# Kernel optimization log

Hardware: AMD Instinct MI355X
Metric: run time of the kernel (lower is better)

The kernel has to match this reference:

```python
import jax, jax.numpy as jnp
import numpy as np
from jax import lax

B, T = 8192, 128
HID = 64


def setup_inputs() -> dict:
    key = jax.random.key(0)
    ks = jax.random.split(key, 16)
    actor_ids = jax.random.randint(ks[0], (B, T), 0, 7, dtype=jnp.int32)
    action_ids = jax.random.randint(ks[1], (B, T), 0, 4, dtype=jnp.int32)
    street_ids = jax.random.randint(ks[2], (B, T), 0, 5, dtype=jnp.int32)
    bet_fraction = jax.random.uniform(ks[3], (B, T, 1), dtype=jnp.float32)
    # prefix-valid mask from random lengths (some zero-length rows)
    lengths = jax.random.randint(ks[4], (B,), 0, T + 1)
    valid_mask = jnp.arange(T)[None, :] < lengths[:, None]  # [B,T] bool
    s = 0.1
    params = {
        "E_actor": jax.random.normal(ks[5], (7, 8), jnp.float32) * s,
        "E_action": jax.random.normal(ks[6], (4, 8), jnp.float32) * s,
        "E_street": jax.random.normal(ks[7], (5, 4), jnp.float32) * s,
        "W_proj": jax.random.normal(ks[8], (32, 21), jnp.float32) * s,
        "b_proj": jax.random.normal(ks[9], (32,), jnp.float32) * s,
        "W_ih": jax.random.normal(ks[10], (3 * HID, 32), jnp.float32) * s,
        "W_hh": jax.random.normal(ks[11], (3 * HID, HID), jnp.float32) * s,
        "b_ih": jax.random.normal(ks[12], (3 * HID,), jnp.float32) * s,
        "b_hh": jax.random.normal(ks[13], (3 * HID,), jnp.float32) * s,
    }
    return dict(actor_ids=actor_ids, action_ids=action_ids, street_ids=street_ids,
                bet_fraction=bet_fraction, valid_mask=valid_mask, **params)


def reference(actor_ids, action_ids, street_ids, bet_fraction, valid_mask,
              E_actor, E_action, E_street, W_proj, b_proj,
              W_ih, W_hh, b_ih, b_hh):
    # embed + concat -> [B,T,21]
    feats = jnp.concatenate([E_actor[actor_ids], E_action[action_ids],
                             E_street[street_ids], bet_fraction], axis=-1)
    x = feats @ W_proj.T + b_proj                      # [B,T,32]
    # precompute input-side GRU gates for all timesteps: [B,T,3H]
    xg = x @ W_ih.T + b_ih
    xg_t = jnp.swapaxes(xg, 0, 1)                      # [T,B,3H]
    m_t = jnp.swapaxes(valid_mask, 0, 1)               # [T,B]

    def step(h, inp):
        xg_i, m = inp
        hg = h @ W_hh.T + b_hh                         # [B,3H]
        xr, xz, xn = jnp.split(xg_i, 3, axis=-1)
        hr, hz, hn = jnp.split(hg, 3, axis=-1)
        r = jax.nn.sigmoid(xr + hr)
        z = jax.nn.sigmoid(xz + hz)
        n = jnp.tanh(xn + r * hn)
        h_new = (1.0 - z) * n + z * h
        # only advance hidden state while t < length (prefix-valid mask);
        # final carry equals the GRU hidden at the last valid step, and rows
        # with length 0 stay at the zero init (matches torch masking).
        h = jnp.where(m[:, None], h_new, h)
        return h, None

    h0 = jnp.zeros((x.shape[0], HID), dtype=x.dtype)
    h_final, _ = lax.scan(step, h0, (xg_t, m_t))
    return h_final
```

## Files before the change

### kernel.cpp

```cpp
#include <hip/hip_runtime.h>

#define HID 64
#define TT  128
#define NROWS 8192
#define NGRP (NROWS / 16)
#define LOG2E 1.44269504088896f

typedef _Float16 half8 __attribute__((ext_vector_type(8)));
typedef float    f32x4 __attribute__((ext_vector_type(4)));

#define WS_WF    0
#define WS_WHH   12288
#define WS_BA    36864
#define WS_BX    37376
#define WS_BH    37632
#define WS_EMB   37888
#define WS_LROW  38176
#define WS_ORDER 70944

__global__ __launch_bounds__(256) void prep(
    const float* __restrict__ E_actor, const float* __restrict__ E_action,
    const float* __restrict__ E_street, const float* __restrict__ W_proj,
    const float* __restrict__ b_proj, const float* __restrict__ W_ih,
    const float* __restrict__ b_ih, const float* __restrict__ W_hh,
    const float* __restrict__ b_hh, const int* __restrict__ mask,
    char* __restrict__ ws)
{
    const int j = threadIdx.x;
    if (blockIdx.x != 64) {
        int* Lrow = (int*)(ws + WS_LROW);
        const int wv = j >> 6, ln = j & 63;
        const int r0 = blockIdx.x * 128;
        for (int i = 0; i < 32; i++) {
            const int row = r0 + i * 4 + wv, base = row * TT;
            const int m0 = mask[base + ln], m1 = mask[base + 64 + ln];
            const int L = __popcll(__ballot(m0 != 0)) + __popcll(__ballot(m1 != 0));
            if (ln == 0) Lrow[row] = L;
        }
        return;
    }

    _Float16* WF  = (_Float16*)(ws + WS_WF);
    _Float16* WHH = (_Float16*)(ws + WS_WHH);
    float*    BA  = (float*)(ws + WS_BA);
    float*    BX  = (float*)(ws + WS_BX);
    float*    BH  = (float*)(ws + WS_BH);
    _Float16* EMB = (_Float16*)(ws + WS_EMB);

    __shared__ float wfs[192][32];
    if (j < 192) {
        float wf[21];
        #pragma unroll
        for (int m = 0; m < 21; m++) wf[m] = 0.f;
        float bf = b_ih[j];
        for (int k = 0; k < 32; k++) {
            float w = W_ih[j * 32 + k];
            bf += w * b_proj[k];
            #pragma unroll
            for (int m = 0; m < 21; m++) wf[m] += w * W_proj[k * 21 + m];
        }
        const float s = (j < 128) ? LOG2E : 2.f * LOG2E;
        #pragma unroll
        for (int m = 0; m < 21; m++) wfs[j][m] = wf[m] * s;
        #pragma unroll
        for (int m = 21; m < 32; m++) wfs[j][m] = 0.f;
        if (j < 128) BA[j] = (bf + b_hh[j]) * LOG2E;
        else { BX[j - 128] = bf * 2.f * LOG2E; BH[j - 128] = b_hh[j] * 2.f * LOG2E; }
    }
    if (j < 17 * 8) {
        int r = j >> 3, m = j & 7;
        float v = 0.f;
        if (r < 7)       v = E_actor[r * 8 + m];
        else if (r < 11) v = E_action[(r - 7) * 8 + m];
        else if (r < 16) v = (m < 4) ? E_street[(r - 11) * 4 + m] : 0.f;
        EMB[j] = (_Float16)v;
    }
    __syncthreads();

    for (int idx = j; idx < 12 * 64; idx += 256) {
        const int T = idx >> 6, lane = idx & 63;
        const int g3 = T >> 2, w = T & 3, m16 = lane & 15, kq = lane >> 4;
        const int jr = g3 * 64 + w * 16 + m16;
        _Float16 v[8];
        #pragma unroll
        for (int m = 0; m < 8; m++) v[m] = (_Float16)wfs[jr][kq * 8 + m];
        *(uint4*)&WF[idx * 8] = *(uint4*)v;
    }
    for (int idx = j; idx < 12 * 2 * 64; idx += 256) {
        const int T = idx >> 7, rem = idx & 127, kt = rem >> 6, lane = rem & 63;
        const int g3 = T >> 2, w = T & 3, m16 = lane & 15, kq = lane >> 4;
        const int jr = g3 * 64 + w * 16 + m16;
        const int kbase = kt * 32 + kq * 8;
        const float s = (jr < 128) ? LOG2E : 2.f * LOG2E;
        _Float16 v[8];
        #pragma unroll
        for (int m = 0; m < 8; m++) v[m] = (_Float16)(W_hh[jr * HID + kbase + m] * s);
        *(uint4*)&WHH[((T * 2 + kt) * 64 + lane) * 8] = *(uint4*)v;
    }
}

__global__ __launch_bounds__(256) void sort_rows(
    const int* __restrict__ Lrow, int* __restrict__ order)
{
    __shared__ int hist[TT + 1];
    __shared__ int pref[TT + 1];
    const int tid = threadIdx.x;
    if (tid <= TT) hist[tid] = 0;
    __syncthreads();
    int rnk[NROWS / 256], Ls[NROWS / 256];
    #pragma unroll 4
    for (int i = 0; i < NROWS / 256; i++) {
        const int r = i * 256 + tid;
        const int L = Lrow[r];
        Ls[i] = L;
        rnk[i] = atomicAdd(&hist[L], 1);
    }
    __syncthreads();
    if (tid == 0) {
        int run = 0;
        for (int i = 0; i <= TT; i++) { pref[i] = run; run += hist[i]; }
    }
    __syncthreads();
    #pragma unroll 4
    for (int i = 0; i < NROWS / 256; i++) {
        const int r = i * 256 + tid;
        order[pref[Ls[i]] + rnk[i]] = r;
    }
}

__global__ __launch_bounds__(256, 2) void gru_mfma(
    const int* __restrict__ actor_ids, const int* __restrict__ action_ids,
    const int* __restrict__ street_ids, const float* __restrict__ bet,
    const char* __restrict__ ws, const int* __restrict__ order,
    const int* __restrict__ Lrow, float* __restrict__ out)
{
    const _Float16* WF  = (const _Float16*)(ws + WS_WF);
    const _Float16* WHH = (const _Float16*)(ws + WS_WHH);
    const float*    BA  = (const float*)(ws + WS_BA);
    const float*    BX  = (const float*)(ws + WS_BX);
    const float*    BH  = (const float*)(ws + WS_BH);
    const _Float16* EMB = (const _Float16*)(ws + WS_EMB);

    __shared__ int pb[TT][17];
    __shared__ __align__(16) _Float16 hb[2][16][72];
    __shared__ __align__(16) _Float16 embl[144];

    const int tid = threadIdx.x;
    const int wv  = tid >> 6;
    const int l   = tid & 63;
    const int q   = l >> 4;
    const int n   = l & 15;

    const int b = blockIdx.x;
    const int g = (b & 1) ? (NGRP - 1 - (b >> 1)) : (b >> 1);

    for (int i = tid; i < 136; i += 256) embl[i] = EMB[i];
    for (int i = tid; i < 2 * 16 * 72 / 2; i += 256) ((int*)hb)[i] = 0;
    {
        const int r = tid >> 4, tl = tid & 15;
        const int rowr = order[g * 16 + r];
        const int base = rowr * TT;
        #pragma unroll
        for (int i = 0; i < 8; i++) {
            const int t = tl + 16 * i;
            const int a = actor_ids[base + t], c = action_ids[base + t];
            const int s = street_ids[base + t];
            const _Float16 f16 = (_Float16)bet[base + t];
            const unsigned fb = (unsigned)*(const unsigned short*)&f16;
            pb[t][r] = (int)(a | (c << 3) | (s << 5) | (fb << 16));
        }
    }

    half8 Af[3], Ah[3][2];
    #pragma unroll
    for (int g3 = 0; g3 < 3; g3++) {
        const int T = g3 * 4 + wv;
        Af[g3]    = *(const half8*)&WF[(T * 64 + l) * 8];
        Ah[g3][0] = *(const half8*)&WHH[((T * 2 + 0) * 64 + l) * 8];
        Ah[g3][1] = *(const half8*)&WHH[((T * 2 + 1) * 64 + l) * 8];
    }
    f32x4 biasR, biasZ, biasX, biasH;
    #pragma unroll
    for (int e = 0; e < 4; e++) {
        const int idx = 16 * wv + 4 * q + e;
        biasR[e] = BA[idx];
        biasZ[e] = BA[64 + idx];
        biasX[e] = BX[idx];
        biasH[e] = BH[idx];
    }

    const int myrow = order[g * 16 + n];
    const int Ln    = Lrow[myrow];
    const int Lmax  = __shfl(Ln, 15);
    const bool isq2 = (q == 2);
    const int sh = (q == 1) ? 3 : (q == 2) ? 5 : 0;
    const int mk = (q == 1) ? 3 : (q == 3) ? 0 : 7;
    const int of = (q == 1) ? 7 : (q == 2) ? 11 : (q == 3) ? 16 : 0;

    float h[4] = {0.f, 0.f, 0.f, 0.f};

    __syncthreads();

    f32x4 xR, xZ, xX;
    {
        const int p = pb[0][n];
        const int eidx = ((p >> sh) & mk) + of;
        half8 Bf = *(const half8*)&embl[eidx * 8];
        uint4* bu = (uint4*)&Bf;
        bu->z = isq2 ? ((unsigned)p >> 16) : bu->z;
        xR = __builtin_amdgcn_mfma_f32_16x16x32_f16(Af[0], Bf, biasR, 0, 0, 0);
        xZ = __builtin_amdgcn_mfma_f32_16x16x32_f16(Af[1], Bf, biasZ, 0, 0, 0);
        xX = __builtin_amdgcn_mfma_f32_16x16x32_f16(Af[2], Bf, biasX, 0, 0, 0);
    }

    for (int t = 0; t < Lmax; t++) {
        const int buf = t & 1;
        const half8 Bh0 = *(const half8*)&hb[buf][n][q * 8];
        const half8 Bh1 = *(const half8*)&hb[buf][n][32 + q * 8];
        f32x4 aR = __builtin_amdgcn_mfma_f32_16x16x32_f16(Ah[0][0], Bh0, xR, 0, 0, 0);
        aR = __builtin_amdgcn_mfma_f32_16x16x32_f16(Ah[0][1], Bh1, aR, 0, 0, 0);
        f32x4 aZ = __builtin_amdgcn_mfma_f32_16x16x32_f16(Ah[1][0], Bh0, xZ, 0, 0, 0);
        aZ = __builtin_amdgcn_mfma_f32_16x16x32_f16(Ah[1][1], Bh1, aZ, 0, 0, 0);
        f32x4 aH = __builtin_amdgcn_mfma_f32_16x16x32_f16(Ah[2][0], Bh0, biasH, 0, 0, 0);
        aH = __builtin_amdgcn_mfma_f32_16x16x32_f16(Ah[2][1], Bh1, aH, 0, 0, 0);
        const f32x4 aXc = xX;

        {
            const int tn = (t + 1 < TT) ? t + 1 : TT - 1;
            const int p = pb[tn][n];
            const int eidx = ((p >> sh) & mk) + of;
            half8 Bf = *(const half8*)&embl[eidx * 8];
            uint4* bu = (uint4*)&Bf;
            bu->z = isq2 ? ((unsigned)p >> 16) : bu->z;
            xR = __builtin_amdgcn_mfma_f32_16x16x32_f16(Af[0], Bf, biasR, 0, 0, 0);
            xZ = __builtin_amdgcn_mfma_f32_16x16x32_f16(Af[1], Bf, biasZ, 0, 0, 0);
            xX = __builtin_amdgcn_mfma_f32_16x16x32_f16(Af[2], Bf, biasX, 0, 0, 0);
        }

        const bool live = (t < Ln);
        _Float16 hp[4];
        #pragma unroll
        for (int e = 0; e < 4; e++) {
            const float r = __builtin_amdgcn_rcpf(1.f + __builtin_amdgcn_exp2f(-aR[e]));
            const float z = __builtin_amdgcn_rcpf(1.f + __builtin_amdgcn_exp2f(-aZ[e]));
            const float y2 = aXc[e] + r * aH[e];
            const float nn = 1.f - 2.f * __builtin_amdgcn_rcpf(1.f + __builtin_amdgcn_exp2f(y2));
            const float hv = nn + z * (h[e] - nn);
            h[e] = live ? hv : h[e];
            hp[e] = (_Float16)h[e];
        }
        *(uint2*)&hb[buf ^ 1][n][16 * wv + 4 * q] = *(uint2*)hp;
        __syncthreads();
    }

    float4 o = make_float4(h[0], h[1], h[2], h[3]);
    *(float4*)&out[myrow * HID + 16 * wv + 4 * q] = o;
}

extern "C" void kernel_launch(void* const* d_in, const int* in_sizes, int n_in,
                              void* d_out, int out_size, void* d_ws, size_t ws_size,
                              hipStream_t stream) {
    const int*   actor_ids  = (const int*)d_in[0];
    const int*   action_ids = (const int*)d_in[1];
    const int*   street_ids = (const int*)d_in[2];
    const float* bet        = (const float*)d_in[3];
    const int*   vmask      = (const int*)d_in[4];
    const float* E_actor    = (const float*)d_in[5];
    const float* E_action   = (const float*)d_in[6];
    const float* E_street   = (const float*)d_in[7];
    const float* W_proj     = (const float*)d_in[8];
    const float* b_proj     = (const float*)d_in[9];
    const float* W_ih       = (const float*)d_in[10];
    const float* W_hh       = (const float*)d_in[11];
    const float* b_ih       = (const float*)d_in[12];
    const float* b_hh       = (const float*)d_in[13];
    float*       out        = (float*)d_out;

    char* ws = (char*)d_ws;
    int*  Lrow  = (int*)(ws + WS_LROW);
    int*  order = (int*)(ws + WS_ORDER);

    prep<<<65, 256, 0, stream>>>(E_actor, E_action, E_street, W_proj, b_proj,
                                 W_ih, b_ih, W_hh, b_hh, vmask, ws);
    sort_rows<<<1, 256, 0, stream>>>(Lrow, order);
    gru_mfma<<<NGRP, 256, 0, stream>>>(actor_ids, action_ids, street_ids, bet,
                                       ws, order, Lrow, out);
}
```

Baseline: 175.7 us.

## Fuse prep, sort and GRU into one cooperative kernel with grid syncs

Merges the three launches (prep, single-block sort_rows, gru_mfma) into one cooperative kernel of 512 blocks separated by two grid-wide syncs. Row lengths are computed per block, weight prep is split across blocks 0-2, and the single-block counting sort is replaced by a parallel rank computation in which each row counts how many rows are shorter or tie with a lower index. The aim is to remove launch gaps and the serial single-block sort. In exchange it adds grid.sync costs and redundant O(N^2) rank comparisons per block, and it requires all 512 blocks to be co-resident.

Measured after the change: 379.3 us. 116% more time.

```diff
diff --git a/kernel.cpp b/kernel.cpp
--- a/kernel.cpp
+++ b/kernel.cpp
@@ -1,4 +1,7 @@
 #include <hip/hip_runtime.h>
+#include <hip/hip_cooperative_groups.h>
+
+namespace cg = cooperative_groups;
 
 #define HID 64
 #define TT  128
@@ -18,27 +21,18 @@
 #define WS_LROW  38176
 #define WS_ORDER 70944
 
-__global__ __launch_bounds__(256) void prep(
+__global__ __launch_bounds__(256, 2) void gru_all(
+    const int* __restrict__ actor_ids, const int* __restrict__ action_ids,
+    const int* __restrict__ street_ids, const float* __restrict__ bet,
+    const int* __restrict__ mask,
     const float* __restrict__ E_actor, const float* __restrict__ E_action,
     const float* __restrict__ E_street, const float* __restrict__ W_proj,
     const float* __restrict__ b_proj, const float* __restrict__ W_ih,
     const float* __restrict__ b_ih, const float* __restrict__ W_hh,
-    const float* __restrict__ b_hh, const int* __restrict__ mask,
-    char* __restrict__ ws)
+    const float* __restrict__ b_hh,
+    char* __restrict__ ws, float* __restrict__ out)
 {
-    const int j = threadIdx.x;
-    if (blockIdx.x != 64) {
-        int* Lrow = (int*)(ws + WS_LROW);
-        const int wv = j >> 6, ln = j & 63;
-        const int r0 = blockIdx.x * 128;
-        for (int i = 0; i < 32; i++) {
-            const int row = r0 + i * 4 + wv, base = row * TT;
-            const int m0 = mask[base + ln], m1 = mask[base + 64 + ln];
-            const int L = __popcll(__ballot(m0 != 0)) + __popcll(__ballot(m1 != 0));
-            if (ln == 0) Lrow[row] = L;
-        }
-        return;
-    }
+    cg::grid_group grid = cg::this_grid();
 
     _Float16* WF  = (_Float16*)(ws + WS_WF);
     _Float16* WHH = (_Float16*)(ws + WS_WHH);
@@ -46,112 +40,129 @@
     float*    BX  = (float*)(ws + WS_BX);
     float*    BH  = (float*)(ws + WS_BH);
     _Float16* EMB = (_Float16*)(ws + WS_EMB);
-
-    __shared__ float wfs[192][32];
-    if (j < 192) {
-        float wf[21];
+    int*      Lrow  = (int*)(ws + WS_LROW);
+    int*      order = (int*)(ws + WS_ORDER);
+
+    __shared__ __align__(16) char arena[25728];
+    __shared__ __align__(16) _Float16 embl[144];
+
+    const int tid = threadIdx.x;
+    const int b   = blockIdx.x;
+
+    {
+        int* part = (int*)arena;
+        const int r = tid >> 4, tl = tid & 15;
+        const int base = (b * 16 + r) * TT;
+        int cnt = 0;
         #pragma unroll
-        for (int m = 0; m < 21; m++) wf[m] = 0.f;
-        float bf = b_ih[j];
-        for (int k = 0; k < 32; k++) {
-            float w = W_ih[j * 32 + k];
-            bf += w * b_proj[k];
-            #pragma unroll
-            for (int m = 0; m < 21; m++) wf[m] += w * W_proj[k * 21 + m];
-        }
-        const float s = (j < 128) ? LOG2E : 2.f * LOG2E;
-        #pragma unroll
-        for (int m = 0; m < 21; m++) wfs[j][m] = wf[m] * s;
-        #pragma unroll
-        for (int m = 21; m < 32; m++) wfs[j][m] = 0.f;
-        if (j < 128) BA[j] = (bf + b_hh[j]) * LOG2E;
-        else { BX[j - 128] = bf * 2.f * LOG2E; BH[j - 128] = b_hh[j] * 2.f * LOG2E; }
-    }
-    if (j < 17 * 8) {
-        int r = j >> 3, m = j & 7;
-        float v = 0.f;
-        if (r < 7)       v = E_actor[r * 8 + m];
-        else if (r < 11) v = E_action[(r - 7) * 8 + m];
-        else if (r < 16) v = (m < 4) ? E_street[(r - 11) * 4 + m] : 0.f;
-        EMB[j] = (_Float16)v;
-    }
-    __syncthreads();
-
-    for (int idx = j; idx < 12 * 64; idx += 256) {
-        const int T = idx >> 6, lane = idx & 63;
-        const int g3 = T >> 2, w = T & 3, m16 = lane & 15, kq = lane >> 4;
-        const int jr = g3 * 64 + w * 16 + m16;
-        _Float16 v[8];
-        #pragma unroll
-        for (int m = 0; m < 8; m++) v[m] = (_Float16)wfs[jr][kq * 8 + m];
-        *(uint4*)&WF[idx * 8] = *(uint4*)v;
-    }
-    for (int idx = j; idx < 12 * 2 * 64; idx += 256) {
-        const int T = idx >> 7, rem = idx & 127, kt = rem >> 6, lane = rem & 63;
-        const int g3 = T >> 2, w = T & 3, m16 = lane & 15, kq = lane >> 4;
-        const int jr = g3 * 64 + w * 16 + m16;
-        const int kbase = kt * 32 + kq * 8;
-        const float s = (jr < 128) ? LOG2E : 2.f * LOG2E;
-        _Float16 v[8];
-        #pragma unroll
-        for (int m = 0; m < 8; m++) v[m] = (_Float16)(W_hh[jr * HID + kbase + m] * s);
-        *(uint4*)&WHH[((T * 2 + kt) * 64 + lane) * 8] = *(uint4*)v;
-    }
-}
-
-__global__ __launch_bounds__(256) void sort_rows(
-    const int* __restrict__ Lrow, int* __restrict__ order)
-{
-    __shared__ int hist[TT + 1];
-    __shared__ int pref[TT + 1];
-    const int tid = threadIdx.x;
-    if (tid <= TT) hist[tid] = 0;
-    __syncthreads();
-    int rnk[NROWS / 256], Ls[NROWS / 256];
-    #pragma unroll 4
-    for (int i = 0; i < NROWS / 256; i++) {
-        const int r = i * 256 + tid;
-        const int L = Lrow[r];
-        Ls[i] = L;
-        rnk[i] = atomicAdd(&hist[L], 1);
-    }
-    __syncthreads();
-    if (tid == 0) {
-        int run = 0;
-        for (int i = 0; i <= TT; i++) { pref[i] = run; run += hist[i]; }
-    }
-    __syncthreads();
-    #pragma unroll 4
-    for (int i = 0; i < NROWS / 256; i++) {
-        const int r = i * 256 + tid;
-        order[pref[Ls[i]] + rnk[i]] = r;
-    }
-}
-
-__global__ __launch_bounds__(256, 2) void gru_mfma(
-    const int* __restrict__ actor_ids, const int* __restrict__ action_ids,
-    const int* __restrict__ street_ids, const float* __restrict__ bet,
-    const char* __restrict__ ws, const int* __restrict__ order,
-    const int* __restrict__ Lrow, float* __restrict__ out)
-{
-    const _Float16* WF  = (const _Float16*)(ws + WS_WF);
-    const _Float16* WHH = (const _Float16*)(ws + WS_WHH);
-    const float*    BA  = (const float*)(ws + WS_BA);
-    const float*    BX  = (const float*)(ws + WS_BX);
-    const float*    BH  = (const float*)(ws + WS_BH);
-    const _Float16* EMB = (const _Float16*)(ws + WS_EMB);
-
-    __shared__ int pb[TT][17];
-    __shared__ __align__(16) _Float16 hb[2][16][72];
-    __shared__ __align__(16) _Float16 embl[144];
-
-    const int tid = threadIdx.x;
-    const int wv  = tid >> 6;
-    const int l   = tid & 63;
-    const int q   = l >> 4;
-    const int n   = l & 15;
-
-    const int b = blockIdx.x;
+        for (int i = 0; i < 8; i++) cnt += (mask[base + tl + 16 * i] != 0);
+        part[r * 16 + tl] = cnt;
+        __syncthreads();
+        if (tid < 16) {
+            int L = 0;
+            #pragma unroll
+            for (int i = 0; i < 16; i++) L += part[tid * 16 + i];
+            Lrow[b * 16 + tid] = L;
+        }
+        __syncthreads();
+    }
+
+    if (b == 0) {
+        float* wfs = (float*)arena;
+        const int j = tid;
+        if (j < 192) {
+            float wf[21];
+            #pragma unroll
+            for (int m = 0; m < 21; m++) wf[m] = 0.f;
+            float bf = b_ih[j];
+            for (int k = 0; k < 32; k++) {
+                float w = W_ih[j * 32 + k];
+                bf += w * b_proj[k];
+                #pragma unroll
+                for (int m = 0; m < 21; m++) wf[m] += w * W_proj[k * 21 + m];
+            }
+            const float s = (j < 128) ? LOG2E : 2.f * LOG2E;
+            #pragma unroll
+            for (int m = 0; m < 21; m++) wfs[j * 32 + m] = wf[m] * s;
+            #pragma unroll
+            for (int m = 21; m < 32; m++) wfs[j * 32 + m] = 0.f;
+            if (j < 128) BA[j] = (bf + b_hh[j]) * LOG2E;
+            else { BX[j - 128] = bf * 2.f * LOG2E; BH[j - 128] = b_hh[j] * 2.f * LOG2E; }
+        }
+        __syncthreads();
+        for (int idx = tid; idx < 12 * 64; idx += 256) {
+            const int T = idx >> 6, lane = idx & 63;
+            const int g3 = T >> 2, w = T & 3, m16 = lane & 15, kq = lane >> 4;
+            const int jr = g3 * 64 + w * 16 + m16;
+            _Float16 v[8];
+            #pragma unroll
+            for (int m = 0; m < 8; m++) v[m] = (_Float16)wfs[jr * 32 + kq * 8 + m];
+            *(uint4*)&WF[idx * 8] = *(uint4*)v;
+        }
+    } else if (b == 1) {
+        for (int idx = tid; idx < 12 * 2 * 64; idx += 256) {
+            const int T = idx >> 7, rem = idx & 127, kt = rem >> 6, lane = rem & 63;
+            const int g3 = T >> 2, w = T & 3, m16 = lane & 15, kq = lane >> 4;
+            const int jr = g3 * 64 + w * 16 + m16;
+            const int kbase = kt * 32 + kq * 8;
+            const float s = (jr < 128) ? LOG2E : 2.f * LOG2E;
+            _Float16 v[8];
+            #pragma unroll
+            for (int m = 0; m < 8; m++) v[m] = (_Float16)(W_hh[jr * HID + kbase + m] * s);
+            *(uint4*)&WHH[((T * 2 + kt) * 64 + lane) * 8] = *(uint4*)v;
+        }
+    } else if (b == 2) {
+        if (tid < 17 * 8) {
+            int r = tid >> 3, m = tid & 7;
+            float v = 0.f;
+            if (r < 7)       v = E_actor[r * 8 + m];
+            else if (r < 11) v = E_action[(r - 7) * 8 + m];
+            else if (r < 16) v = (m < 4) ? E_street[(r - 11) * 4 + m] : 0.f;
+            EMB[tid] = (_Float16)v;
+        }
+    }
+    __threadfence();
+    grid.sync();
+
+    {
+        int* Lds = (int*)arena;
+        int* pB  = (int*)(arena + 8192);
+        const int j  = tid & 15, tp = tid >> 4;
+        const int myr = b * 16 + j;
+        const int Lj  = Lrow[myr];
+        int cnt = 0;
+        for (int c = 0; c < 4; c++) {
+            for (int i = tid; i < 2048; i += 256) Lds[i] = Lrow[c * 2048 + i];
+            __syncthreads();
+            const int kb = c * 2048 + tp * 128;
+            #pragma unroll 4
+            for (int k = 0; k < 128; k++) {
+                const int Lk = Lds[tp * 128 + k];
+                const int kg = kb + k;
+                cnt += (Lk < Lj) | ((Lk == Lj) & (kg < myr));
+            }
+            __syncthreads();
+        }
+        pB[j * 16 + tp] = cnt;
+        __syncthreads();
+        if (tid < 16) {
+            int pos = 0;
+            #pragma unroll
+            for (int i = 0; i < 16; i++) pos += pB[tid * 16 + i];
+            order[pos] = b * 16 + tid;
+        }
+    }
+    __threadfence();
+    grid.sync();
+
+    int*      pb = (int*)arena;
+    _Float16* hb = (_Float16*)(arena + 8704);
+
+    const int wv = tid >> 6;
+    const int l  = tid & 63;
+    const int q  = l >> 4;
+    const int n  = l & 15;
+
     const int g = (b & 1) ? (NGRP - 1 - (b >> 1)) : (b >> 1);
 
     for (int i = tid; i < 136; i += 256) embl[i] = EMB[i];
@@ -167,7 +178,7 @@
             const int s = street_ids[base + t];
             const _Float16 f16 = (_Float16)bet[base + t];
             const unsigned fb = (unsigned)*(const unsigned short*)&f16;
-            pb[t][r] = (int)(a | (c << 3) | (s << 5) | (fb << 16));
+            pb[t * 17 + r] = (int)(a | (c << 3) | (s << 5) | (fb << 16));
         }
     }
 
@@ -203,7 +214,7 @@
 
     f32x4 xR, xZ, xX;
     {
-        const int p = pb[0][n];
+        const int p = pb[0 * 17 + n];
         const int eidx = ((p >> sh) & mk) + of;
         half8 Bf = *(const half8*)&embl[eidx * 8];
         uint4* bu = (uint4*)&Bf;
@@ -215,8 +226,8 @@
 
     for (int t = 0; t < Lmax; t++) {
         const int buf = t & 1;
-        const half8 Bh0 = *(const half8*)&hb[buf][n][q * 8];
-        const half8 Bh1 = *(const half8*)&hb[buf][n][32 + q * 8];
+        const half8 Bh0 = *(const half8*)&hb[(buf * 16 + n) * 72 + q * 8];
+        const half8 Bh1 = *(const half8*)&hb[(buf * 16 + n) * 72 + 32 + q * 8];
         f32x4 aR = __builtin_amdgcn_mfma_f32_16x16x32_f16(Ah[0][0], Bh0, xR, 0, 0, 0);
         aR = __builtin_amdgcn_mfma_f32_16x16x32_f16(Ah[0][1], Bh1, aR, 0, 0, 0);
         f32x4 aZ = __builtin_amdgcn_mfma_f32_16x16x32_f16(Ah[1][0], Bh0, xZ, 0, 0, 0);
@@ -227,7 +238,7 @@
 
         {
             const int tn = (t + 1 < TT) ? t + 1 : TT - 1;
-            const int p = pb[tn][n];
+            const int p = pb[tn * 17 + n];
             const int eidx = ((p >> sh) & mk) + of;
             half8 Bf = *(const half8*)&embl[eidx * 8];
             uint4* bu = (uint4*)&Bf;
@@ -249,7 +260,7 @@
             h[e] = live ? hv : h[e];
             hp[e] = (_Float16)h[e];
         }
-        *(uint2*)&hb[buf ^ 1][n][16 * wv + 4 * q] = *(uint2*)hp;
+        *(uint2*)&hb[((buf ^ 1) * 16 + n) * 72 + 16 * wv + 4 * q] = *(uint2*)hp;
         __syncthreads();
     }
 
@@ -271,18 +282,18 @@
     const float* W_proj     = (const float*)d_in[8];
     const float* b_proj     = (const float*)d_in[9];
     const float* W_ih       = (const float*)d_in[10];
+    const float* b_ih       = (const float*)d_in[12];
     const float* W_hh       = (const float*)d_in[11];
-    const float* b_ih       = (const float*)d_in[12];
     const float* b_hh       = (const float*)d_in[13];
     float*       out        = (float*)d_out;
-
-    char* ws = (char*)d_ws;
-    int*  Lrow  = (int*)(ws + WS_LROW);
-    int*  order = (int*)(ws + WS_ORDER);
-
-    prep<<<65, 256, 0, stream>>>(E_actor, E_action, E_street, W_proj, b_proj,
-                                 W_ih, b_ih, W_hh, b_hh, vmask, ws);
-    sort_rows<<<1, 256, 0, stream>>>(Lrow, order);
-    gru_mfma<<<NGRP, 256, 0, stream>>>(actor_ids, action_ids, street_ids, bet,
-                                       ws, order, Lrow, out);
+    char*        ws         = (char*)d_ws;
+
+    void* args[] = {
+        (void*)&actor_ids, (void*)&action_ids, (void*)&street_ids, (void*)&bet,
+        (void*)&vmask, (void*)&E_actor, (void*)&E_action, (void*)&E_street,
+        (void*)&W_proj, (void*)&b_proj, (void*)&W_ih, (void*)&b_ih,
+        (void*)&W_hh, (void*)&b_hh, (void*)&ws, (void*)&out
+    };
+    hipLaunchCooperativeKernel((const void*)gru_all, dim3(NGRP), dim3(256),
+                               args, 0, stream);
 }
```

## Replace single-block counting sort with parallel rank-by-comparison sort

Applied to the files above, without the earlier changes.

The single-workgroup histogram sort of rows by length becomes a rank sort spread over 512 workgroups. Each workgroup computes the stable rank of its 16 rows by comparing them against all 8192 lengths staged through shared memory, then scatters them into the order array. This removes a serial single-block stage in front of the GRU kernel, at the cost of O(N^2) comparisons and repeated global reads of the length array.

Measured after the change: 181.9 us. 3.5% more time.

```diff
diff --git a/kernel.cpp b/kernel.cpp
--- a/kernel.cpp
+++ b/kernel.cpp
@@ -99,32 +99,36 @@
     }
 }
 
-__global__ __launch_bounds__(256) void sort_rows(
+__global__ __launch_bounds__(256) void psort(
     const int* __restrict__ Lrow, int* __restrict__ order)
 {
-    __shared__ int hist[TT + 1];
-    __shared__ int pref[TT + 1];
+    __shared__ int Lds[2048];
+    __shared__ int pB[16][16];
     const int tid = threadIdx.x;
-    if (tid <= TT) hist[tid] = 0;
+    const int b   = blockIdx.x;
+    const int j = tid & 15, tp = tid >> 4;
+    const int myr = b * 16 + j;
+    const int Lj  = Lrow[myr];
+    int cnt = 0;
+    for (int c = 0; c < 4; c++) {
+        for (int i = tid; i < 2048; i += 256) Lds[i] = Lrow[c * 2048 + i];
+        __syncthreads();
+        const int kb = c * 2048 + tp * 128;
+        #pragma unroll 4
+        for (int k = 0; k < 128; k++) {
+            const int Lk = Lds[tp * 128 + k];
+            const int kg = kb + k;
+            cnt += (Lk < Lj) | ((Lk == Lj) & (kg < myr));
+        }
+        __syncthreads();
+    }
+    pB[j][tp] = cnt;
     __syncthreads();
-    int rnk[NROWS / 256], Ls[NROWS / 256];
-    #pragma unroll 4
-    for (int i = 0; i < NROWS / 256; i++) {
-        const int r = i * 256 + tid;
-        const int L = Lrow[r];
-        Ls[i] = L;
-        rnk[i] = atomicAdd(&hist[L], 1);
-    }
-    __syncthreads();
-    if (tid == 0) {
-        int run = 0;
-        for (int i = 0; i <= TT; i++) { pref[i] = run; run += hist[i]; }
-    }
-    __syncthreads();
-    #pragma unroll 4
-    for (int i = 0; i < NROWS / 256; i++) {
-        const int r = i * 256 + tid;
-        order[pref[Ls[i]] + rnk[i]] = r;
+    if (tid < 16) {
+        int pos = 0;
+        #pragma unroll
+        for (int i = 0; i < 16; i++) pos += pB[tid][i];
+        order[pos] = b * 16 + tid;
     }
 }
 
@@ -282,7 +286,7 @@
 
     prep<<<65, 256, 0, stream>>>(E_actor, E_action, E_street, W_proj, b_proj,
                                  W_ih, b_ih, W_hh, b_hh, vmask, ws);
-    sort_rows<<<1, 256, 0, stream>>>(Lrow, order);
+    psort<<<NGRP, 256, 0, stream>>>(Lrow, order);
     gru_mfma<<<NGRP, 256, 0, stream>>>(actor_ids, action_ids, street_ids, bet,
                                        ws, order, Lrow, out);
 }
```

## Fold length sort into GRU kernel, dropping the single-block sort launch

Applied to the files above, without the earlier changes.

Removes the separate one-block sort_rows kernel. Each GRU block now builds its own length histogram over all rows, gathers the candidate rows whose length bucket overlaps its 16-row slot, bitonic-sorts them in shared memory and picks its rows. The prep kernel's mask-length count is also rewritten to use strided per-thread counts and a shared-memory reduction in place of wave ballots. This removes a serial single-block launch and its dependency, but every one of the 512 blocks now reads all 8192 lengths and does extra shared-memory work, and more than 512 candidates in one bucket would overflow the candidate buffer.

After: 189.1 us. +7.6%, slower.

```diff
diff --git a/kernel.cpp b/kernel.cpp
--- a/kernel.cpp
+++ b/kernel.cpp
@@ -16,7 +16,6 @@
 #define WS_BH    37632
 #define WS_EMB   37888
 #define WS_LROW  38176
-#define WS_ORDER 70944
 
 __global__ __launch_bounds__(256) void prep(
     const float* __restrict__ E_actor, const float* __restrict__ E_action,
@@ -29,13 +28,23 @@
     const int j = threadIdx.x;
     if (blockIdx.x != 64) {
         int* Lrow = (int*)(ws + WS_LROW);
-        const int wv = j >> 6, ln = j & 63;
-        const int r0 = blockIdx.x * 128;
-        for (int i = 0; i < 32; i++) {
-            const int row = r0 + i * 4 + wv, base = row * TT;
-            const int m0 = mask[base + ln], m1 = mask[base + 64 + ln];
-            const int L = __popcll(__ballot(m0 != 0)) + __popcll(__ballot(m1 != 0));
-            if (ln == 0) Lrow[row] = L;
+        __shared__ int part[16][16];
+        const int r = j >> 4, tl = j & 15;
+        for (int it = 0; it < 8; it++) {
+            const int row = blockIdx.x * 128 + it * 16 + r;
+            const int base = row * TT;
+            int cnt = 0;
+            #pragma unroll
+            for (int i = 0; i < 8; i++) cnt += (mask[base + tl + 16 * i] != 0);
+            part[r][tl] = cnt;
+            __syncthreads();
+            if (j < 16) {
+                int L = 0;
+                #pragma unroll
+                for (int i = 0; i < 16; i++) L += part[j][i];
+                Lrow[blockIdx.x * 128 + it * 16 + j] = L;
+            }
+            __syncthreads();
         }
         return;
     }
@@ -99,40 +108,11 @@
     }
 }
 
-__global__ __launch_bounds__(256) void sort_rows(
-    const int* __restrict__ Lrow, int* __restrict__ order)
-{
-    __shared__ int hist[TT + 1];
-    __shared__ int pref[TT + 1];
-    const int tid = threadIdx.x;
-    if (tid <= TT) hist[tid] = 0;
-    __syncthreads();
-    int rnk[NROWS / 256], Ls[NROWS / 256];
-    #pragma unroll 4
-    for (int i = 0; i < NROWS / 256; i++) {
-        const int r = i * 256 + tid;
-        const int L = Lrow[r];
-        Ls[i] = L;
-        rnk[i] = atomicAdd(&hist[L], 1);
-    }
-    __syncthreads();
-    if (tid == 0) {
-        int run = 0;
-        for (int i = 0; i <= TT; i++) { pref[i] = run; run += hist[i]; }
-    }
-    __syncthreads();
-    #pragma unroll 4
-    for (int i = 0; i < NROWS / 256; i++) {
-        const int r = i * 256 + tid;
-        order[pref[Ls[i]] + rnk[i]] = r;
-    }
-}
-
 __global__ __launch_bounds__(256, 2) void gru_mfma(
     const int* __restrict__ actor_ids, const int* __restrict__ action_ids,
     const int* __restrict__ street_ids, const float* __restrict__ bet,
-    const char* __restrict__ ws, const int* __restrict__ order,
-    const int* __restrict__ Lrow, float* __restrict__ out)
+    const char* __restrict__ ws, const int* __restrict__ Lrow,
+    float* __restrict__ out)
 {
     const _Float16* WF  = (const _Float16*)(ws + WS_WF);
     const _Float16* WHH = (const _Float16*)(ws + WS_WHH);
@@ -141,9 +121,21 @@
     const float*    BH  = (const float*)(ws + WS_BH);
     const _Float16* EMB = (const _Float16*)(ws + WS_EMB);
 
-    __shared__ int pb[TT][17];
-    __shared__ __align__(16) _Float16 hb[2][16][72];
+    __shared__ __align__(16) union {
+        struct {
+            int hist[129];
+            int pref[129];
+            int cand[512];
+            int ncand;
+        } s;
+        struct {
+            int pb[TT][17];
+            __align__(16) _Float16 hb[2][16][72];
+        } c;
+    } A;
     __shared__ __align__(16) _Float16 embl[144];
+    __shared__ int ordr[16];
+    __shared__ int Lw[16];
 
     const int tid = threadIdx.x;
     const int wv  = tid >> 6;
@@ -153,13 +145,56 @@
 
     const int b = blockIdx.x;
     const int g = (b & 1) ? (NGRP - 1 - (b >> 1)) : (b >> 1);
+    const int s0 = g * 16;
 
     for (int i = tid; i < 136; i += 256) embl[i] = EMB[i];
-    for (int i = tid; i < 2 * 16 * 72 / 2; i += 256) ((int*)hb)[i] = 0;
+
+    for (int i = tid; i < 129; i += 256) A.s.hist[i] = 0;
+    if (tid == 0) A.s.ncand = 0;
+    __syncthreads();
+    for (int i = tid; i < NROWS; i += 256) atomicAdd(&A.s.hist[Lrow[i]], 1);
+    __syncthreads();
+    if (tid == 0) {
+        int run = 0;
+        for (int i = 0; i < 129; i++) { A.s.pref[i] = run; run += A.s.hist[i]; }
+    }
+    __syncthreads();
+    for (int i = tid; i < NROWS; i += 256) {
+        const int L = Lrow[i];
+        if (A.s.pref[L] < s0 + 16 && A.s.pref[L] + A.s.hist[L] > s0) {
+            const int k = atomicAdd(&A.s.ncand, 1);
+            if (k < 512) A.s.cand[k] = (L << 13) | i;
+        }
+    }
+    __syncthreads();
+    const int nc = A.s.ncand;
+    for (int i = tid; i < 512; i += 256) if (i >= nc) A.s.cand[i] = 0x7fffffff;
+    for (int k = 2; k <= 512; k <<= 1) {
+        for (int jj = k >> 1; jj > 0; jj >>= 1) {
+            __syncthreads();
+            for (int w = tid; w < 512; w += 256) {
+                const int ixj = w ^ jj;
+                if (ixj > w) {
+                    const int a = A.s.cand[w], bb = A.s.cand[ixj];
+                    const bool up = ((w & k) == 0);
+                    if ((a > bb) == up) { A.s.cand[w] = bb; A.s.cand[ixj] = a; }
+                }
+            }
+        }
+    }
+    __syncthreads();
+    if (tid < 16) {
+        const int off = s0 - A.s.pref[A.s.cand[0] >> 13];
+        const int key = A.s.cand[off + tid];
+        ordr[tid] = key & 8191;
+        Lw[tid]   = key >> 13;
+    }
+    __syncthreads();
+
+    for (int i = tid; i < 2 * 16 * 72 / 2; i += 256) ((int*)A.c.hb)[i] = 0;
     {
         const int r = tid >> 4, tl = tid & 15;
-        const int rowr = order[g * 16 + r];
-        const int base = rowr * TT;
+        const int base = ordr[r] * TT;
         #pragma unroll
         for (int i = 0; i < 8; i++) {
             const int t = tl + 16 * i;
@@ -167,7 +202,7 @@
             const int s = street_ids[base + t];
             const _Float16 f16 = (_Float16)bet[base + t];
             const unsigned fb = (unsigned)*(const unsigned short*)&f16;
-            pb[t][r] = (int)(a | (c << 3) | (s << 5) | (fb << 16));
+            A.c.pb[t][r] = (int)(a | (c << 3) | (s << 5) | (fb << 16));
         }
     }
 
@@ -189,21 +224,20 @@
         biasH[e] = BH[idx];
     }
 
-    const int myrow = order[g * 16 + n];
-    const int Ln    = Lrow[myrow];
-    const int Lmax  = __shfl(Ln, 15);
+    const int myrow = ordr[n];
+    const int Ln    = Lw[n];
+    const int Lmax  = Lw[15];
     const bool isq2 = (q == 2);
     const int sh = (q == 1) ? 3 : (q == 2) ? 5 : 0;
     const int mk = (q == 1) ? 3 : (q == 3) ? 0 : 7;
     const int of = (q == 1) ? 7 : (q == 2) ? 11 : (q == 3) ? 16 : 0;
 
     float h[4] = {0.f, 0.f, 0.f, 0.f};
-
     __syncthreads();
 
     f32x4 xR, xZ, xX;
     {
-        const int p = pb[0][n];
+        const int p = A.c.pb[0][n];
         const int eidx = ((p >> sh) & mk) + of;
         half8 Bf = *(const half8*)&embl[eidx * 8];
         uint4* bu = (uint4*)&Bf;
@@ -215,8 +249,8 @@
 
     for (int t = 0; t < Lmax; t++) {
         const int buf = t & 1;
-        const half8 Bh0 = *(const half8*)&hb[buf][n][q * 8];
-        const half8 Bh1 = *(const half8*)&hb[buf][n][32 + q * 8];
+        const half8 Bh0 = *(const half8*)&A.c.hb[buf][n][q * 8];
+        const half8 Bh1 = *(const half8*)&A.c.hb[buf][n][32 + q * 8];
         f32x4 aR = __builtin_amdgcn_mfma_f32_16x16x32_f16(Ah[0][0], Bh0, xR, 0, 0, 0);
         aR = __builtin_amdgcn_mfma_f32_16x16x32_f16(Ah[0][1], Bh1, aR, 0, 0, 0);
         f32x4 aZ = __builtin_amdgcn_mfma_f32_16x16x32_f16(Ah[1][0], Bh0, xZ, 0, 0, 0);
@@ -227,7 +261,7 @@
 
         {
             const int tn = (t + 1 < TT) ? t + 1 : TT - 1;
-            const int p = pb[tn][n];
+            const int p = A.c.pb[tn][n];
             const int eidx = ((p >> sh) & mk) + of;
             half8 Bf = *(const half8*)&embl[eidx * 8];
             uint4* bu = (uint4*)&Bf;
@@ -249,7 +283,7 @@
             h[e] = live ? hv : h[e];
             hp[e] = (_Float16)h[e];
         }
-        *(uint2*)&hb[buf ^ 1][n][16 * wv + 4 * q] = *(uint2*)hp;
+        *(uint2*)&A.c.hb[buf ^ 1][n][16 * wv + 4 * q] = *(uint2*)hp;
         __syncthreads();
     }
 
@@ -277,12 +311,10 @@
     float*       out        = (float*)d_out;
 
     char* ws = (char*)d_ws;
-    int*  Lrow  = (int*)(ws + WS_LROW);
-    int*  order = (int*)(ws + WS_ORDER);
+    int*  Lrow = (int*)(ws + WS_LROW);
 
     prep<<<65, 256, 0, stream>>>(E_actor, E_action, E_street, W_proj, b_proj,
                                  W_ih, b_ih, W_hh, b_hh, vmask, ws);
-    sort_rows<<<1, 256, 0, stream>>>(Lrow, order);
     gru_mfma<<<NGRP, 256, 0, stream>>>(actor_ids, action_ids, street_ids, bet,
-                                       ws, order, Lrow, out);
+                                       ws, Lrow, out);
 }
```
